# Kernel tuning notes

Hardware: AMD Instinct MI355X
Metric: run time of the kernel (lower is better)

Reference implementation:

```python
import jax, jax.numpy as jnp
import numpy as np

M, K, N = 8192, 4096, 4096
DIV = 1.0 / (127.0 * 127.0)


def setup_inputs() -> dict:
    key = jax.random.key(0)
    k1, k2, k3, k4, k5 = jax.random.split(key, 5)
    x = jax.random.randint(k1, (M, K), -127, 128, dtype=jnp.int8)
    weight_int8 = jax.random.randint(k2, (N, K), -127, 128, dtype=jnp.int8)
    scale_x = jnp.abs(jax.random.normal(k3, (M,), dtype=jnp.float32)) * 0.01
    scale_w = jnp.abs(jax.random.normal(k4, (N,), dtype=jnp.float32)) * 0.01
    bias = (jax.random.normal(k5, (N,), dtype=jnp.float32) * 0.01).astype(jnp.float16)
    return {"x": x, "scale_x": scale_x, "weight_int8": weight_int8,
            "scale_w": scale_w, "bias": bias}


def reference(x, scale_x, weight_int8, scale_w, bias):
    # int8 GEMM with int32 accumulation: [M,K] @ [K,N]
    acc = jax.lax.dot_general(
        x, weight_int8.T,
        dimension_numbers=(((1,), (0,)), ((), ())),
        preferred_element_type=jnp.int32,
    ).astype(jnp.float32)
    # fused rowwise/colwise dequant + bias, cast to fp16
    out = acc * DIV * scale_x[:, None] * scale_w[None, :] + bias.astype(jnp.float32)[None, :]
    return out.astype(jnp.float16)
```

## Files before the change

### kernel.cpp

```cpp
#include <hip/hip_runtime.h>
#include <hip/hip_fp16.h>
#include <cstdint>
#include <cstddef>

#define M_DIM 8192
#define N_DIM 4096
#define K_DIM 4096

typedef int v4i __attribute__((ext_vector_type(4)));

__global__ __launch_bounds__(256) void pack_i32_to_i8(const int* __restrict__ srcX,
                                                      uint32_t* __restrict__ dstX,
                                                      const int* __restrict__ srcW,
                                                      uint32_t* __restrict__ dstW,
                                                      int nx4, int ntot) {
    int i = blockIdx.x * 256 + threadIdx.x;
    if (i >= ntot) return;
    const int* s;
    uint32_t*  d;
    int j;
    if (i < nx4) { s = srcX; d = dstX; j = i; }
    else         { s = srcW; d = dstW; j = i - nx4; }
    int4 a = ((const int4*)s)[j];
#if __has_builtin(__builtin_amdgcn_perm)
    uint32_t lo = __builtin_amdgcn_perm((uint32_t)a.y, (uint32_t)a.x, 0x0400);
    uint32_t hi = __builtin_amdgcn_perm((uint32_t)a.w, (uint32_t)a.z, 0x0400);
    d[j] = __builtin_amdgcn_perm(hi, lo, 0x05040100);
#else
    d[j] = (uint32_t)(a.x & 0xff) | ((uint32_t)(a.y & 0xff) << 8) |
           ((uint32_t)(a.z & 0xff) << 16) | ((uint32_t)a.w << 24);
#endif
}

__device__ __forceinline__ void gload_lds16(const int8_t* g, int8_t* l) {
    __builtin_amdgcn_global_load_lds(
        (const __attribute__((address_space(1))) void*)g,
        (__attribute__((address_space(3))) void*)l, 16, 0, 0);
}


#define VMW(n) asm volatile("s_waitcnt vmcnt(" #n ")" ::: "memory")

#define KTILE(KT, DO_STAGE, VMSTMT, DO_SYNC)                                  \
    do {                                                                      \
        const int8_t* bufA = lds + ((KT) & 3) * 32768;                        \
        const int8_t* bufB = bufA + 16384;                                    \
        v4i af[4], bf[4], a2[4];                                              \
        _Pragma("unroll")                                                     \
        for (int i = 0; i < 4; ++i) {                                         \
            af[i] = *(const v4i*)(bufA + aoff + i * 1024);                    \
            bf[i] = *(const v4i*)(bufB + boff + i * 1024);                    \
        }                                                                     \
        _Pragma("unroll")                                                     \
        for (int i = 0; i < 4; ++i)                                           \
            a2[i] = *(const v4i*)(bufA + aoff + 4096 + i * 1024);             \
        if (DO_STAGE) {                                                       \
            int8_t* sAb = lds + (((KT) + 3) & 3) * 32768;                     \
            gload_lds16(gA0 + ((KT) + 3) * 64, sAb + ldsoff);                 \
            gload_lds16(gA1 + ((KT) + 3) * 64, sAb + ldsoff + 8192);          \
            gload_lds16(gB0 + ((KT) + 3) * 64, sAb + 16384 + ldsoff);         \
            gload_lds16(gB1 + ((KT) + 3) * 64, sAb + 16384 + ldsoff + 8192);  \
        }                                                                     \
        __builtin_amdgcn_s_setprio(1);                                        \
        _Pragma("unroll")                                                     \
        for (int mi = 0; mi < 4; ++mi) {                                      \
            _Pragma("unroll")                                                 \
            for (int ni = 0; ni < 4; ++ni)                                    \
                acc[mi][ni] = __builtin_amdgcn_mfma_i32_16x16x64_i8(          \
                    af[mi], bf[ni], acc[mi][ni], 0, 0, 0);                    \
        }                                                                     \
        _Pragma("unroll")                                                     \
        for (int mi = 0; mi < 4; ++mi) {                                      \
            _Pragma("unroll")                                                 \
            for (int ni = 0; ni < 4; ++ni)                                    \
                acc[4 + mi][ni] = __builtin_amdgcn_mfma_i32_16x16x64_i8(      \
                    a2[mi], bf[ni], acc[4 + mi][ni], 0, 0, 0);                \
        }                                                                     \
        __builtin_amdgcn_s_setprio(0);                                        \
        if (DO_SYNC) {                                                        \
            __builtin_amdgcn_sched_barrier(0);                                \
            VMSTMT;                                                           \
            __builtin_amdgcn_s_barrier();                                     \
            __builtin_amdgcn_sched_barrier(0);                                \
        }                                                                     \
    } while (0)

__global__ __launch_bounds__(512, 2) void gemm_i8_dq(const int8_t* __restrict__ A,
                                                     const int8_t* __restrict__ W,
                                                     const float* __restrict__ sx,
                                                     const float* __restrict__ sw,
                                                     const float* __restrict__ bias,
                                                     float* __restrict__ out) {
    __shared__ __attribute__((aligned(16))) int8_t lds[131072];

    const int t    = threadIdx.x;
    const int lane = t & 63;
    const int w    = t >> 6;
    const int wm   = w >> 2;
    const int wn   = w & 3;

    const int flat = blockIdx.y * 16 + blockIdx.x;
    const int xcd  = flat & 7;
    const int idx  = flat >> 3;
    const int bm   = (xcd >> 1) * 8 + (idx & 7);
    const int bn   = (xcd & 1) * 8 + (idx >> 3);

    const int srow   = t >> 2;
    const int rot    = (srow >> 1) & 3;
    const int gchunk = ((t & 3) + rot) & 3;
    const int scol   = gchunk * 16;
    const int8_t* gA0 = A + (size_t)(bm * 256 + srow) * K_DIM + scol;
    const int8_t* gA1 = gA0 + (size_t)128 * K_DIM;
    const int8_t* gB0 = W + (size_t)(bn * 256 + srow) * K_DIM + scol;
    const int8_t* gB1 = gB0 + (size_t)128 * K_DIM;
    const int ldsoff = t * 16;

    const int rho  = lane & 15;
    const int p16  = (((lane >> 4) - (rho >> 1)) & 3) * 16;
    const int aoff = (wm * 128 + rho) * 64 + p16;
    const int boff = (wn * 64 + rho) * 64 + p16;

    v4i acc[8][4];
    const v4i vzero = {0, 0, 0, 0};
#pragma unroll
    for (int mi = 0; mi < 8; mi++)
#pragma unroll
        for (int ni = 0; ni < 4; ni++) acc[mi][ni] = vzero;

#pragma unroll
    for (int pt = 0; pt < 3; ++pt) {
        int8_t* bufA = lds + pt * 32768;
        int8_t* bufB = bufA + 16384;
        gload_lds16(gA0 + pt * 64, bufA + ldsoff);
        gload_lds16(gA1 + pt * 64, bufA + ldsoff + 8192);
        gload_lds16(gB0 + pt * 64, bufB + ldsoff);
        gload_lds16(gB1 + pt * 64, bufB + ldsoff + 8192);
    }
    VMW(8);
    __builtin_amdgcn_s_barrier();
    __builtin_amdgcn_sched_barrier(0);

    for (int kt = 0; kt < 61; ++kt) KTILE(kt, true, VMW(8), true);
    KTILE(61, false, VMW(4), true);
    KTILE(62, false, VMW(0), true);
    KTILE(63, false, ((void)0), false);

    const float DIVF = (float)(1.0 / (127.0 * 127.0));
    const int col0 = bn * 256 + wn * 64 + (lane & 15);
    const int row0 = bm * 256 + wm * 128 + (lane >> 4) * 4;

    float swv[4], bv[4];
#pragma unroll
    for (int ni = 0; ni < 4; ni++) {
        swv[ni] = sw[col0 + ni * 16];
        bv[ni]  = bias[col0 + ni * 16];
    }

#pragma unroll
    for (int mi = 0; mi < 8; mi++) {
#pragma unroll
        for (int r = 0; r < 4; r++) {
            const int row = row0 + mi * 16 + r;
            const float xs = sx[row];
#pragma unroll
            for (int ni = 0; ni < 4; ni++) {
                float v = __fmul_rn((float)acc[mi][ni][r], DIVF);
                v = __fmul_rn(v, xs);
                v = __fmul_rn(v, swv[ni]);
                v = __fadd_rn(v, bv[ni]);
                out[(size_t)row * N_DIM + col0 + ni * 16] = __half2float(__float2half(v));
            }
        }
    }
}

extern "C" void kernel_launch(void* const* d_in, const int* in_sizes, int n_in,
                              void* d_out, int out_size, void* d_ws, size_t ws_size,
                              hipStream_t stream) {
    const int*   x_i32 = (const int*)d_in[0];
    const float* sx    = (const float*)d_in[1];
    const int*   w_i32 = (const int*)d_in[2];
    const float* sw    = (const float*)d_in[3];
    const float* bias  = (const float*)d_in[4];
    float* out = (float*)d_out;

    uint8_t* xb = (uint8_t*)d_ws;
    uint8_t* wb = (uint8_t*)d_ws + (size_t)M_DIM * K_DIM;

    const int nx4  = (M_DIM * K_DIM) / 4;
    const int nw4  = (N_DIM * K_DIM) / 4;
    const int ntot = nx4 + nw4;
    pack_i32_to_i8<<<(ntot + 255) / 256, 256, 0, stream>>>(
        x_i32, (uint32_t*)xb, w_i32, (uint32_t*)wb, nx4, ntot);

    dim3 grid(N_DIM / 256, M_DIM / 256);
    gemm_i8_dq<<<grid, 512, 0, stream>>>((const int8_t*)xb, (const int8_t*)wb,
                                         sx, sw, bias, out);
}
```

Before: 386.6 us.

## Double-buffer LDS fragments in registers to overlap LDS reads with MFMA

The K loop is restructured so the LDS fragments for tile kt+1 are loaded into a second register set while the MFMAs for tile kt run from the first set. The loop is unrolled by two so the register sets swap roles, and the vmcnt waits and epilogue are rewritten to keep the four-slot LDS ring correct. This hides LDS read latency behind matrix math. The cost is 48 extra live VGPRs per thread, which at the 2-blocks-per-CU launch bound could cause spills or lower occupancy.

```diff
diff --git a/kernel.cpp b/kernel.cpp
--- a/kernel.cpp
+++ b/kernel.cpp
@@ -41,43 +41,51 @@
 
 #define VMW(n) asm volatile("s_waitcnt vmcnt(" #n ")" ::: "memory")
 
-#define KTILE(KT, DO_STAGE, VMSTMT, DO_SYNC)                                  \
+#define LOADF(DA, DB, DC, KT1)                                                \
     do {                                                                      \
-        const int8_t* bufA = lds + ((KT) & 3) * 32768;                        \
-        const int8_t* bufB = bufA + 16384;                                    \
-        v4i af[4], bf[4], a2[4];                                              \
+        const int8_t* _b = lds + ((KT1) & 3) * 32768;                         \
         _Pragma("unroll")                                                     \
         for (int i = 0; i < 4; ++i) {                                         \
-            af[i] = *(const v4i*)(bufA + aoff + i * 1024);                    \
-            bf[i] = *(const v4i*)(bufB + boff + i * 1024);                    \
+            DA[i] = *(const v4i*)(_b + aoff + i * 1024);                      \
+            DB[i] = *(const v4i*)(_b + 16384 + boff + i * 1024);              \
+            DC[i] = *(const v4i*)(_b + aoff + 4096 + i * 1024);               \
         }                                                                     \
+    } while (0)
+
+#define STAGE(KT3)                                                            \
+    do {                                                                      \
+        int8_t* _s = lds + ((KT3) & 3) * 32768;                               \
+        gload_lds16(gA0 + (KT3) * 64, _s + ldsoff);                           \
+        gload_lds16(gA1 + (KT3) * 64, _s + ldsoff + 8192);                    \
+        gload_lds16(gB0 + (KT3) * 64, _s + 16384 + ldsoff);                   \
+        gload_lds16(gB1 + (KT3) * 64, _s + 16384 + ldsoff + 8192);            \
+    } while (0)
+
+#define MFMA32(CA, CB, CC)                                                    \
+    __builtin_amdgcn_s_setprio(1);                                            \
+    _Pragma("unroll")                                                         \
+    for (int mi = 0; mi < 4; ++mi) {                                          \
         _Pragma("unroll")                                                     \
-        for (int i = 0; i < 4; ++i)                                           \
-            a2[i] = *(const v4i*)(bufA + aoff + 4096 + i * 1024);             \
-        if (DO_STAGE) {                                                       \
-            int8_t* sAb = lds + (((KT) + 3) & 3) * 32768;                     \
-            gload_lds16(gA0 + ((KT) + 3) * 64, sAb + ldsoff);                 \
-            gload_lds16(gA1 + ((KT) + 3) * 64, sAb + ldsoff + 8192);          \
-            gload_lds16(gB0 + ((KT) + 3) * 64, sAb + 16384 + ldsoff);         \
-            gload_lds16(gB1 + ((KT) + 3) * 64, sAb + 16384 + ldsoff + 8192);  \
-        }                                                                     \
-        __builtin_amdgcn_s_setprio(1);                                        \
+        for (int ni = 0; ni < 4; ++ni)                                        \
+            acc[mi][ni] = __builtin_amdgcn_mfma_i32_16x16x64_i8(              \
+                CA[mi], CB[ni], acc[mi][ni], 0, 0, 0);                        \
+    }                                                                         \
+    _Pragma("unroll")                                                         \
+    for (int mi = 0; mi < 4; ++mi) {                                          \
         _Pragma("unroll")                                                     \
-        for (int mi = 0; mi < 4; ++mi) {                                      \
-            _Pragma("unroll")                                                 \
-            for (int ni = 0; ni < 4; ++ni)                                    \
-                acc[mi][ni] = __builtin_amdgcn_mfma_i32_16x16x64_i8(          \
-                    af[mi], bf[ni], acc[mi][ni], 0, 0, 0);                    \
-        }                                                                     \
-        _Pragma("unroll")                                                     \
-        for (int mi = 0; mi < 4; ++mi) {                                      \
-            _Pragma("unroll")                                                 \
-            for (int ni = 0; ni < 4; ++ni)                                    \
-                acc[4 + mi][ni] = __builtin_amdgcn_mfma_i32_16x16x64_i8(      \
-                    a2[mi], bf[ni], acc[4 + mi][ni], 0, 0, 0);                \
-        }                                                                     \
-        __builtin_amdgcn_s_setprio(0);                                        \
-        if (DO_SYNC) {                                                        \
+        for (int ni = 0; ni < 4; ++ni)                                        \
+            acc[4 + mi][ni] = __builtin_amdgcn_mfma_i32_16x16x64_i8(          \
+                CC[mi], CB[ni], acc[4 + mi][ni], 0, 0, 0);                    \
+    }                                                                         \
+    __builtin_amdgcn_s_setprio(0);
+
+#define ITER(KT, CA, CB, CC, NA, NB, NC, DOREAD, DOSTAGE, VMSTMT, DOSYNC)     \
+    do {                                                                      \
+        if (DOREAD) LOADF(NA, NB, NC, (KT) + 1);                              \
+        if (DOSTAGE) STAGE((KT) + 3);                                         \
+        __builtin_amdgcn_sched_barrier(0);       \
+        MFMA32(CA, CB, CC);                                                   \
+        if (DOSYNC) {                                                         \
             __builtin_amdgcn_sched_barrier(0);                                \
             VMSTMT;                                                           \
             __builtin_amdgcn_s_barrier();                                     \
@@ -127,23 +135,29 @@
 #pragma unroll
         for (int ni = 0; ni < 4; ni++) acc[mi][ni] = vzero;
 
+    v4i pA[4], pB[4], pC[4], qA[4], qB[4], qC[4];
+
 #pragma unroll
     for (int pt = 0; pt < 3; ++pt) {
         int8_t* bufA = lds + pt * 32768;
-        int8_t* bufB = bufA + 16384;
         gload_lds16(gA0 + pt * 64, bufA + ldsoff);
         gload_lds16(gA1 + pt * 64, bufA + ldsoff + 8192);
-        gload_lds16(gB0 + pt * 64, bufB + ldsoff);
-        gload_lds16(gB1 + pt * 64, bufB + ldsoff + 8192);
-    }
-    VMW(8);
+        gload_lds16(gB0 + pt * 64, bufA + 16384 + ldsoff);
+        gload_lds16(gB1 + pt * 64, bufA + 16384 + ldsoff + 8192);
+    }
+    VMW(4);
     __builtin_amdgcn_s_barrier();
     __builtin_amdgcn_sched_barrier(0);
-
-    for (int kt = 0; kt < 61; ++kt) KTILE(kt, true, VMW(8), true);
-    KTILE(61, false, VMW(4), true);
-    KTILE(62, false, VMW(0), true);
-    KTILE(63, false, ((void)0), false);
+    LOADF(pA, pB, pC, 0);
+
+    for (int kt = 0; kt < 60; kt += 2) {
+        ITER(kt,     pA, pB, pC, qA, qB, qC, true, true, VMW(4), true);
+        ITER(kt + 1, qA, qB, qC, pA, pB, pC, true, true, VMW(4), true);
+    }
+    ITER(60, pA, pB, pC, qA, qB, qC, true,  true,  VMW(4),  true);
+    ITER(61, qA, qB, qC, pA, pB, pC, true,  false, VMW(0),  true);
+    ITER(62, pA, pB, pC, qA, qB, qC, true,  false, ((void)0), false);
+    ITER(63, qA, qB, qC, pA, pB, pC, false, false, ((void)0), false);
 
     const float DIVF = (float)(1.0 / (127.0 * 127.0));
     const int col0 = bn * 256 + wn * 64 + (lane & 15);
```

After: 383.8 us. Within noise of the previous version (-0.7%).
